# Optimization experiments

Hardware: AMD Instinct MI355X
Metric: run time of the kernel (lower is better)

## Reference

```python
import jax, jax.numpy as jnp
import numpy as np

BATCH, K, DIM = 512, 65536, 768

def _l2norm(x, axis=-1, eps=1e-12):
    return x / jnp.maximum(jnp.linalg.norm(x, axis=axis, keepdims=True), eps)

def setup_inputs() -> dict:
    key = jax.random.key(0)
    ks = jax.random.split(key, 8)
    s = 1.0 / np.sqrt(2 * DIM)
    return {
        "img_features": jax.random.normal(ks[0], (BATCH, DIM), jnp.float32),
        "txt_features": jax.random.normal(ks[1], (BATCH, DIM), jnp.float32),
        # queue buffers are L2-normalized at init in the torch module
        "queue_img": _l2norm(jax.random.normal(ks[2], (K, DIM), jnp.float32)),
        "queue_txt": _l2norm(jax.random.normal(ks[3], (K, DIM), jnp.float32)),
        "W_diff": jax.random.normal(ks[4], (2 * DIM, DIM), jnp.float32) * s,
        "b_diff": jnp.zeros((DIM,), jnp.float32),
        "W_comb": jax.random.normal(ks[5], (2 * DIM, DIM), jnp.float32) * s,
        "b_comb": jnp.zeros((DIM,), jnp.float32),
        "logit_scale": jnp.full((1,), 100.0, jnp.float32),  # clip logit_scale.exp()
    }

def reference(img_features, txt_features, queue_img, queue_txt,
              W_diff, b_diff, W_comb, b_comb, logit_scale):
    # normalize encoder outputs
    img_f = _l2norm(img_features)          # [n, c]
    txt_f = _l2norm(txt_features)          # [n, c]
    # brute-force cosine retrieval against the text queue
    retrieval_mat = jnp.einsum('nc,kc->nk', img_f, queue_txt)  # [n, K]
    ind_similar = jnp.argmax(retrieval_mat, axis=-1)           # [n]
    t_similar = queue_txt[ind_similar]                          # gather [n, c]
    # diff_net_q: concat -> linear -> relu
    diff = jax.nn.relu(jnp.concatenate([txt_f, t_similar], -1) @ W_diff + b_diff)
    # combine_net_q: concat -> linear
    combined = jnp.concatenate([img_f, diff], -1) @ W_comb + b_comb
    scale = jnp.mean(logit_scale)
    logits = scale * jnp.einsum('nc,kc->nk', combined, queue_img)  # [n, K]
    # dequeue/enqueue: scatter batch rows into the queue at ptr=0
    new_queue_img = jax.lax.dynamic_update_slice(queue_img, img_f, (0, 0))
    new_queue_txt = jax.lax.dynamic_update_slice(queue_txt, txt_f, (0, 0))
    return logits, ind_similar, new_queue_img, new_queue_txt
```

## Files before the change

### kernel.cpp

```cpp
#include <hip/hip_runtime.h>
#include <stdint.h>
#include <stddef.h>

#define BATCH 512
#define NQ    65536
#define DIM   768
#define DIM2  1536
#define CONVB 1024

typedef __attribute__((ext_vector_type(4))) float f32x4;
typedef __attribute__((ext_vector_type(4))) unsigned short u16x4;
typedef __attribute__((ext_vector_type(8))) unsigned short u16x8;
typedef __attribute__((ext_vector_type(8))) __bf16 bf16x8;

static __device__ __forceinline__ unsigned short f2bf(float x){
    unsigned int u = __float_as_uint(x);
    unsigned int r = ((u >> 16) & 1u) + 0x7fffu;
    return (unsigned short)((u + r) >> 16);
}
static __device__ __forceinline__ float bf2f(unsigned short h){
    return __uint_as_float(((unsigned int)h) << 16);
}

struct T2 { float v1, v2; int i1, i2; };
static __device__ __forceinline__ void t2_add(T2& t, float v, int i){
    if (v > t.v1 || (v == t.v1 && i < t.i1)) { t.v2 = t.v1; t.i2 = t.i1; t.v1 = v; t.i1 = i; }
    else if (v > t.v2 || (v == t.v2 && i < t.i2)) { t.v2 = v; t.i2 = i; }
}
static __device__ __forceinline__ T2 t2_init(){ T2 t; t.v1 = -3.4e38f; t.v2 = -3.4e38f; t.i1 = 0x7fffffff; t.i2 = 0x7fffffff; return t; }

__global__ __launch_bounds__(256) void prep_all(
    const float* __restrict__ img, const float* __restrict__ txt,
    const float* __restrict__ qtxt, const float* __restrict__ qimg,
    const float* __restrict__ Wd, const float* __restrict__ Wc,
    unsigned short* __restrict__ bthi, unsigned short* __restrict__ bihi,
    float* __restrict__ img_f, float* __restrict__ txt_f,
    unsigned short* __restrict__ X2hi, unsigned short* __restrict__ X2lo,
    unsigned short* __restrict__ X1hi, unsigned short* __restrict__ X1lo,
    float* __restrict__ out2, float* __restrict__ out3,
    float* __restrict__ Td, float* __restrict__ Tc)
{
    __shared__ float tbuf[32][33];
    __shared__ float red[4];
    const int b = blockIdx.x;
    if (b < 2 * CONVB){
        const bool isT = (b < CONVB);
        const float* __restrict__ src = isT ? qtxt : qimg;
        unsigned short* __restrict__ hi = isT ? bthi : bihi;
        const int bb = isT ? b : b - CONVB;
        const size_t n4 = (size_t)NQ * DIM / 4;
        for (size_t i = (size_t)bb * 256 + threadIdx.x; i < n4; i += (size_t)CONVB * 256){
            f32x4 v = ((const f32x4*)src)[i];
            u16x4 h;
            #pragma unroll
            for (int j = 0; j < 4; j++) h[j] = f2bf(v[j]);
            *(u16x4*)(hi + 4*i) = h;
        }
    } else if (b < 2 * CONVB + 2 * BATCH){
        const int b2 = b - 2 * CONVB;
        const bool isimg = (b2 < BATCH);
        const int row = isimg ? b2 : b2 - BATCH;
        const float* src = (isimg ? img : txt) + (size_t)row * DIM;
        float v[3];
        float ss = 0.f;
        #pragma unroll
        for (int i = 0; i < 3; i++){ v[i] = src[threadIdx.x + i*256]; ss += v[i]*v[i]; }
        #pragma unroll
        for (int m = 1; m < 64; m <<= 1) ss += __shfl_xor(ss, m);
        if ((threadIdx.x & 63) == 0) red[threadIdx.x >> 6] = ss;
        __syncthreads();
        float tot = red[0] + red[1] + red[2] + red[3];
        float scale = 1.0f / fmaxf(sqrtf(tot), 1e-12f);
        float* fdst = (isimg ? img_f : txt_f) + (size_t)row * DIM;
        float* odst = (isimg ? out2  : out3 ) + (size_t)row * DIM;
        unsigned short* hid = (isimg ? X2hi : X1hi) + (size_t)row * DIM2;
        unsigned short* lod = (isimg ? X2lo : X1lo) + (size_t)row * DIM2;
        #pragma unroll
        for (int i = 0; i < 3; i++){
            int c = threadIdx.x + i*256;
            float y = v[i] * scale;
            fdst[c] = y; odst[c] = y;
            unsigned short h = f2bf(y);
            hid[c] = h; lod[c] = f2bf(y - bf2f(h));
        }
    } else {
        int t = b - 2 * CONVB - 2 * BATCH;
        const int z = t / 1152; t -= z * 1152;
        const int x = t % 24, y = t / 24;
        const float* W = z ? Wc : Wd;
        float*       T = z ? Tc : Td;
        const int x0 = x * 32, y0 = y * 32;
        const int tx = threadIdx.x & 31, ty = threadIdx.x >> 5;
        #pragma unroll
        for (int i = 0; i < 32; i += 8)
            tbuf[ty + i][tx] = W[(size_t)(y0 + ty + i) * DIM + x0 + tx];
        __syncthreads();
        #pragma unroll
        for (int i = 0; i < 32; i += 8)
            T[(size_t)(x0 + ty + i) * DIM2 + y0 + tx] = tbuf[tx][ty + i];
    }
}

#define EPI_TOP2      0
#define EPI_BIAS_RELU 1
#define EPI_BIAS      2
#define EPI_SCALE     3

template<int EPI, bool WT>
__global__ __launch_bounds__(512, 2) void gemm_big(
    const unsigned short* __restrict__ Ahi, const unsigned short* __restrict__ Alo, int lda,
    const unsigned short* __restrict__ Bhi, const unsigned short* __restrict__ Blo, int ldb,
    int K, int Nout,
    float* __restrict__ outp, const float* __restrict__ scale_ptr, int Mtot,
    float* __restrict__ wt_out)
{
    constexpr int NT = 512;
    constexpr int KS = 64;
    constexpr int HT = 16384;
    constexpr int BUF = 4 * HT;
    __shared__ __align__(16) char lds[2 * BUF];

    const int tid = threadIdx.x, lane = tid & 63, wid = tid >> 6;
    const int wm = wid >> 2, wn = wid & 3;
    const int lr = lane & 15, lg = lane >> 4;
    const int id = blockIdx.x;
    const int l  = (id & 7) * 64 + (id >> 3);
    const int nb = l >> 1, mb = l & 1;
    const int m0 = mb * 256, n0 = nb * 256;

    f32x4 acc[8][4] = {};

    auto stageHT = [&](int T){
        int kind = T & 3, ks = T >> 2;
        char* base = lds + (ks & 1) * BUF + kind * HT;
        const unsigned short* hi = (kind < 2) ? Ahi : Bhi;
        const unsigned short* lo = (kind < 2) ? Alo : Blo;
        int ld = (kind < 2) ? lda : ldb;
        int r0 = ((kind < 2) ? m0 : n0) + (kind & 1) * 128;
        int k0 = ks * KS;
        #pragma unroll
        for (int r = 0; r < 2; r++){
            int G = r * NT + tid, row = G >> 3, slot = G & 7, s0 = slot ^ (row & 7);
            const unsigned short* s = ((s0 < 4) ? hi : lo) + (size_t)(r0 + row) * ld + k0 + (s0 & 3) * 8;
            __builtin_amdgcn_global_load_lds(
                (const __attribute__((address_space(1))) void*)s,
                (__attribute__((address_space(3))) void*)(base + (r * NT + (tid & ~63)) * 16), 16, 0, 0);
        }
    };

    const int xh = (lg ^ (lr & 7)) << 4;
    const int xl = ((4 + lg) ^ (lr & 7)) << 4;

    const int nk = K / KS;
    stageHT(0); stageHT(1); stageHT(2); stageHT(3);
    if (nk > 1){
        stageHT(6); stageHT(7);
        asm volatile("s_waitcnt vmcnt(4)" ::: "memory");
    } else {
        asm volatile("s_waitcnt vmcnt(0)" ::: "memory");
    }
    __syncthreads();

    for (int kt = 0; kt < nk; kt++){
        const char* Ab = lds + (kt & 1) * BUF;
        const char* Bb = Ab + 2 * HT;
        bf16x8 bh[4], bl[4];
        #pragma unroll
        for (int q = 0; q < 4; q++){
            if (q < 2){ if (kt + 1 < nk) stageHT(4 * (kt + 1) + q); }
            else      { if (kt + 2 < nk) stageHT(4 * (kt + 2) + q); }
            if (q == 0){
                #pragma unroll
                for (int nf = 0; nf < 4; nf++){
                    const char* rp = Bb + (wn * 64 + nf * 16 + lr) * 128;
                    bh[nf] = *(const bf16x8*)(rp + xh);
                    bl[nf] = *(const bf16x8*)(rp + xl);
                }
            }
            const char* rp0 = Ab + (wm * 128 + q * 32 + lr) * 128;
            const char* rp1 = rp0 + 16 * 128;
            bf16x8 a0h = *(const bf16x8*)(rp0 + xh);
            bf16x8 a0l = *(const bf16x8*)(rp0 + xl);
            bf16x8 a1h = *(const bf16x8*)(rp1 + xh);
            bf16x8 a1l = *(const bf16x8*)(rp1 + xl);
            asm volatile("s_barrier" ::: "memory");
            asm volatile("s_waitcnt lgkmcnt(0)" ::: "memory");
            __builtin_amdgcn_sched_barrier(0);
            __builtin_amdgcn_s_setprio(1);
            #pragma unroll
            for (int nf = 0; nf < 4; nf++)
                acc[2*q  ][nf] = __builtin_amdgcn_mfma_f32_16x16x32_bf16(a0h, bh[nf], acc[2*q  ][nf], 0, 0, 0);
            #pragma unroll
            for (int nf = 0; nf < 4; nf++)
                acc[2*q+1][nf] = __builtin_amdgcn_mfma_f32_16x16x32_bf16(a1h, bh[nf], acc[2*q+1][nf], 0, 0, 0);
            #pragma unroll
            for (int nf = 0; nf < 4; nf++)
                acc[2*q  ][nf] = __builtin_amdgcn_mfma_f32_16x16x32_bf16(a0l, bl[nf], acc[2*q  ][nf], 0, 0, 0);
            #pragma unroll
            for (int nf = 0; nf < 4; nf++)
                acc[2*q+1][nf] = __builtin_amdgcn_mfma_f32_16x16x32_bf16(a1l, bl[nf], acc[2*q+1][nf], 0, 0, 0);
            __builtin_amdgcn_s_setprio(0);
            if (q == 3){
                if (kt < nk - 2)       asm volatile("s_waitcnt vmcnt(4)" ::: "memory");
                else if (kt == nk - 2) asm volatile("s_waitcnt vmcnt(0)" ::: "memory");
            }
            asm volatile("s_barrier" ::: "memory");
        }
    }

    if constexpr (EPI == EPI_TOP2){
        T2* t2l = (T2*)lds;
        #pragma unroll
        for (int mf = 0; mf < 8; mf++){
            #pragma unroll
            for (int r = 0; r < 4; r++){
                T2 t = t2_init();
                #pragma unroll
                for (int nf = 0; nf < 4; nf++){
                    int gc = n0 + wn * 64 + nf * 16 + lr;
                    t2_add(t, acc[mf][nf][r], gc);
                }
                #pragma unroll
                for (int m = 1; m < 16; m <<= 1){
                    float ov1 = __shfl_xor(t.v1, m), ov2 = __shfl_xor(t.v2, m);
                    int   oi1 = __shfl_xor(t.i1, m), oi2 = __shfl_xor(t.i2, m);
                    t2_add(t, ov1, oi1); t2_add(t, ov2, oi2);
                }
                if (lr == 0){
                    int rowit = wm * 128 + mf * 16 + lg * 4 + r;
                    t2l[wn * 256 + rowit] = t;
                }
            }
        }
        __syncthreads();
        if (tid < 256){
            T2 t = t2l[tid];
            #pragma unroll
            for (int w = 1; w < 4; w++){
                T2 o = t2l[w * 256 + tid];
                t2_add(t, o.v1, o.i1); t2_add(t, o.v2, o.i2);
            }
            f32x4 pk; pk[0] = t.v1; pk[1] = __int_as_float(t.i1); pk[2] = t.v2; pk[3] = __int_as_float(t.i2);
            ((f32x4*)outp)[(size_t)nb * Mtot + (m0 + tid)] = pk;
        }
    } else if constexpr (EPI == EPI_SCALE){
        float sc = scale_ptr[0];
        #pragma unroll
        for (int mf = 0; mf < 8; mf++)
        #pragma unroll
        for (int nf = 0; nf < 4; nf++)
        #pragma unroll
        for (int r = 0; r < 4; r++){
            int grow = m0 + wm * 128 + mf * 16 + lg * 4 + r;
            int gcol = n0 + wn * 64 + nf * 16 + lr;
            outp[(size_t)grow * Nout + gcol] = acc[mf][nf][r] * sc;
        }
    }

    if constexpr (WT){
        if (mb == 0){
            constexpr int PR = DIM / 8;
            for (int t = tid; t < 256 * PR; t += NT){
                int r = n0 + t / PR;
                if (r >= BATCH){
                    int c = (t % PR) * 8;
                    u16x8 hv = *(const u16x8*)(Bhi + (size_t)r * ldb + c);
                    f32x4 f0, f1;
                    #pragma unroll
                    for (int j = 0; j < 4; j++){ f0[j] = bf2f(hv[j]); f1[j] = bf2f(hv[4 + j]); }
                    f32x4* wp = (f32x4*)(wt_out + (size_t)r * DIM + c);
                    wp[0] = f0; wp[1] = f1;
                }
            }
        }
    }
}

template<int BM,int BN,int WGM,int WGN,int EPI>
__global__ __launch_bounds__(WGM*WGN*64) void gemm_small(
    const unsigned short* __restrict__ Ahi, const unsigned short* __restrict__ Alo, int lda,
    const float* __restrict__ B, int ldb, int K,
    const float* __restrict__ bias,
    unsigned short* __restrict__ dsthi, unsigned short* __restrict__ dstlo, int ldd, int dstoff)
{
    constexpr int WM = BM / WGM, WN = BN / WGN;
    constexpr int MF = WM / 16, NF = WN / 16;
    constexpr int NT = WGM * WGN * 64;
    constexpr int ABYTES = BM * 128;
    constexpr int BBYTES = BN * 128;
    constexpr int BUF = ABYTES + BBYTES;
    static_assert(BN * 4 == NT, "");
    static_assert((BM * 8) % NT == 0, "");

    __shared__ __align__(16) char lds[2 * BUF];

    const int tid  = threadIdx.x;
    const int wid  = tid >> 6, lane = tid & 63;
    const int wm   = wid / WGN, wn = wid % WGN;
    const int lr   = lane & 15, lg = lane >> 4;
    const int nb   = blockIdx.x, mb = blockIdx.y;
    const int m0   = mb * BM, n0 = nb * BN;

    f32x4 acc[MF][NF] = {};
    f32x4 breg0, breg1;

    auto stageA = [&](int buf, int k0){
        char* base = lds + buf * BUF;
        constexpr int RA = BM * 8 / NT;
        #pragma unroll
        for (int r = 0; r < RA; r++){
            int G = r * NT + tid;
            int row = G >> 3, slot = G & 7;
            int s0 = slot ^ (row & 7);
            const unsigned short* src = ((s0 < 4) ? Ahi : Alo)
                + (size_t)(m0 + row) * lda + (k0 + (s0 & 3) * 8);
            char* ldst = base + r * NT * 16 + (tid & ~63) * 16;
            __builtin_amdgcn_global_load_lds(
                (const __attribute__((address_space(1))) void*)src,
                (__attribute__((address_space(3))) void*)ldst, 16, 0, 0);
        }
    };
    auto loadB = [&](int kt){
        int k0 = kt * 32;
        int row = tid >> 2, quad = tid & 3;
        const float* bp = B + (size_t)(n0 + row) * ldb + k0 + quad * 8;
        breg0 = *(const f32x4*)bp;
        breg1 = *(const f32x4*)(bp + 4);
    };
    auto writeB = [&](int buf){
        char* base = lds + buf * BUF + ABYTES;
        int row = tid >> 2, quad = tid & 3;
        u16x8 h8, l8;
        #pragma unroll
        for (int j = 0; j < 8; j++){
            float x = (j < 4) ? breg0[j] : breg1[j - 4];
            unsigned short h = f2bf(x);
            h8[j] = h; l8[j] = f2bf(x - bf2f(h));
        }
        int sh = quad ^ (row & 7), sl = (4 + quad) ^ (row & 7);
        *(u16x8*)(base + row * 128 + sh * 16) = h8;
        *(u16x8*)(base + row * 128 + sl * 16) = l8;
    };
    auto compute = [&](int buf){
        const char* Ab = lds + buf * BUF;
        const char* Bb = Ab + ABYTES;
        bf16x8 ah[MF], al[MF], bh[NF], bl[NF];
        #pragma unroll
        for (int mf = 0; mf < MF; mf++){
            int row = wm * WM + mf * 16 + lr;
            const char* rp = Ab + row * 128;
            ah[mf] = *(const bf16x8*)(rp + ((lg ^ (row & 7)) << 4));
            al[mf] = *(const bf16x8*)(rp + (((4 + lg) ^ (row & 7)) << 4));
        }
        #pragma unroll
        for (int nf = 0; nf < NF; nf++){
            int row = wn * WN + nf * 16 + lr;
            const char* rp = Bb + row * 128;
            bh[nf] = *(const bf16x8*)(rp + ((lg ^ (row & 7)) << 4));
            bl[nf] = *(const bf16x8*)(rp + (((4 + lg) ^ (row & 7)) << 4));
        }
        #pragma unroll
        for (int mf = 0; mf < MF; mf++)
        #pragma unroll
        for (int nf = 0; nf < NF; nf++){
            acc[mf][nf] = __builtin_amdgcn_mfma_f32_16x16x32_bf16(ah[mf], bh[nf], acc[mf][nf], 0, 0, 0);
            acc[mf][nf] = __builtin_amdgcn_mfma_f32_16x16x32_bf16(al[mf], bh[nf], acc[mf][nf], 0, 0, 0);
            acc[mf][nf] = __builtin_amdgcn_mfma_f32_16x16x32_bf16(ah[mf], bl[nf], acc[mf][nf], 0, 0, 0);
        }
    };

    stageA(0, 0); loadB(0); writeB(0);
    __syncthreads();
    const int nk = K / 32;
    int cur = 0;
    for (int kt = 0; kt < nk; kt++){
        if (kt + 1 < nk){ stageA(cur ^ 1, (kt + 1) * 32); loadB(kt + 1); }
        compute(cur);
        if (kt + 1 < nk){ writeB(cur ^ 1); }
        __syncthreads();
        cur ^= 1;
    }

    #pragma unroll
    for (int mf = 0; mf < MF; mf++)
    #pragma unroll
    for (int nf = 0; nf < NF; nf++)
    #pragma unroll
    for (int r = 0; r < 4; r++){
        int grow = m0 + wm * WM + mf * 16 + lg * 4 + r;
        int gcol = n0 + wn * WN + nf * 16 + lr;
        float c = acc[mf][nf][r] + bias[gcol];
        if (EPI == EPI_BIAS_RELU) c = fmaxf(c, 0.f);
        unsigned short h = f2bf(c);
        size_t o = (size_t)grow * ldd + dstoff + gcol;
        dsthi[o] = h;
        dstlo[o] = f2bf(c - bf2f(h));
    }
}

__global__ __launch_bounds__(256) void phaseB_kernel(
    const f32x4* __restrict__ top2ws, int ntiles,
    const float* __restrict__ img_f, const float* __restrict__ qtxt,
    float* __restrict__ out_ind,
    unsigned short* __restrict__ X1hi, unsigned short* __restrict__ X1lo)
{
    __shared__ float vals[512];
    __shared__ int   inds[512];
    __shared__ float red[4];
    __shared__ int   redi[4];
    __shared__ int   cands[4];
    __shared__ float cscore[4];
    __shared__ int   finali;
    const int row = blockIdx.x, tid = threadIdx.x;

    if (tid < ntiles){
        f32x4 e = top2ws[(size_t)tid * BATCH + row];
        vals[2*tid]   = e[0]; inds[2*tid]   = __float_as_int(e[1]);
        vals[2*tid+1] = e[2]; inds[2*tid+1] = __float_as_int(e[3]);
    }
    __syncthreads();

    for (int it = 0; it < 4; it++){
        float v = vals[tid]; int i = inds[tid];
        {
            float v2 = vals[tid+256]; int i2 = inds[tid+256];
            if (v2 > v || (v2 == v && i2 < i)){ v = v2; i = i2; }
        }
        #pragma unroll
        for (int m = 1; m < 64; m <<= 1){
            float ov = __shfl_xor(v, m); int oi = __shfl_xor(i, m);
            if (ov > v || (ov == v && oi < i)){ v = ov; i = oi; }
        }
        if ((tid & 63) == 0){ red[tid>>6] = v; redi[tid>>6] = i; }
        __syncthreads();
        if (tid == 0){
            float bv = red[0]; int bi = redi[0];
            #pragma unroll
            for (int w = 1; w < 4; w++)
                if (red[w] > bv || (red[w] == bv && redi[w] < bi)){ bv = red[w]; bi = redi[w]; }
            cands[it] = bi;
        }
        __syncthreads();
        if (inds[tid]     == cands[it]) vals[tid]     = -3.4e38f;
        if (inds[tid+256] == cands[it]) vals[tid+256] = -3.4e38f;
        __syncthreads();
    }

    const float* a = img_f + (size_t)row * DIM;
    float a0 = a[tid], a1 = a[tid + 256], a2 = a[tid + 512];
    for (int c = 0; c < 4; c++){
        const float* bp = qtxt + (size_t)cands[c] * DIM;
        float s = a0 * bp[tid] + a1 * bp[tid + 256] + a2 * bp[tid + 512];
        #pragma unroll
        for (int m = 1; m < 64; m <<= 1) s += __shfl_xor(s, m);
        if ((tid & 63) == 0) red[tid>>6] = s;
        __syncthreads();
        if (tid == 0) cscore[c] = red[0] + red[1] + red[2] + red[3];
        __syncthreads();
    }
    if (tid == 0){
        float bs = cscore[0]; int bi = cands[0];
        #pragma unroll
        for (int c = 1; c < 4; c++)
            if (cscore[c] > bs || (cscore[c] == bs && cands[c] < bi)){ bs = cscore[c]; bi = cands[c]; }
        out_ind[row] = (float)bi;
        finali = bi;
    }
    __syncthreads();

    const float* src = qtxt + (size_t)finali * DIM;
    for (int c = tid; c < DIM; c += 256){
        float x = src[c];
        unsigned short h = f2bf(x);
        X1hi[(size_t)row * DIM2 + DIM + c] = h;
        X1lo[(size_t)row * DIM2 + DIM + c] = f2bf(x - bf2f(h));
    }
}

extern "C" void kernel_launch(void* const* d_in, const int* in_sizes, int n_in,
                              void* d_out, int out_size, void* d_ws, size_t ws_size,
                              hipStream_t stream)
{
    (void)in_sizes; (void)n_in; (void)out_size; (void)ws_size;
    const float* img  = (const float*)d_in[0];
    const float* txt  = (const float*)d_in[1];
    const float* qimg = (const float*)d_in[2];
    const float* qtxt = (const float*)d_in[3];
    const float* Wd   = (const float*)d_in[4];
    const float* bd   = (const float*)d_in[5];
    const float* Wc   = (const float*)d_in[6];
    const float* bc   = (const float*)d_in[7];
    const float* ls   = (const float*)d_in[8];

    float* out0 = (float*)d_out;
    float* out1 = out0 + (size_t)BATCH * NQ;
    float* out2 = out1 + BATCH;
    float* out3 = out2 + (size_t)NQ * DIM;

    char* w = (char*)d_ws;
    auto alloc = [&](size_t bytes){ char* p = w; w += (bytes + 255) & ~(size_t)255; return p; };
    unsigned short* X1hi  = (unsigned short*)alloc((size_t)BATCH * DIM2 * 2);
    unsigned short* X1lo  = (unsigned short*)alloc((size_t)BATCH * DIM2 * 2);
    unsigned short* X2hi  = (unsigned short*)alloc((size_t)BATCH * DIM2 * 2);
    unsigned short* X2lo  = (unsigned short*)alloc((size_t)BATCH * DIM2 * 2);
    unsigned short* combhi= (unsigned short*)alloc((size_t)BATCH * DIM * 2);
    unsigned short* comblo= (unsigned short*)alloc((size_t)BATCH * DIM * 2);
    float* img_f  = (float*)alloc((size_t)BATCH * DIM * 4);
    float* txt_f  = (float*)alloc((size_t)BATCH * DIM * 4);
    float* Td     = (float*)alloc((size_t)DIM * DIM2 * 4);
    float* Tc     = (float*)alloc((size_t)DIM * DIM2 * 4);
    float* top2ws = (float*)alloc((size_t)(NQ / 256) * BATCH * 16);
    unsigned short* Bt_hi = (unsigned short*)alloc((size_t)NQ * DIM * 2);
    unsigned short* Bi_hi = (unsigned short*)alloc((size_t)NQ * DIM * 2);

    prep_all<<<dim3(2 * CONVB + 2 * BATCH + 2304), dim3(256), 0, stream>>>(
        img, txt, qtxt, qimg, Wd, Wc, Bt_hi, Bi_hi,
        img_f, txt_f, X2hi, X2lo, X1hi, X1lo, out2, out3, Td, Tc);

    gemm_big<EPI_TOP2, true><<<dim3(512), dim3(512), 0, stream>>>(
        X2hi, X2hi + 32, DIM2, Bt_hi, Bt_hi + 32, DIM, DIM, NQ, top2ws, nullptr, BATCH, out3);

    phaseB_kernel<<<dim3(BATCH), dim3(256), 0, stream>>>(
        (const f32x4*)top2ws, NQ / 256, img_f, qtxt, out1, X1hi, X1lo);

    gemm_small<64,64,2,2,EPI_BIAS_RELU><<<dim3(DIM / 64, BATCH / 64), dim3(256), 0, stream>>>(
        X1hi, X1lo, DIM2, Td, DIM2, DIM2, bd, X2hi, X2lo, DIM2, DIM);

    gemm_small<64,64,2,2,EPI_BIAS><<<dim3(DIM / 64, BATCH / 64), dim3(256), 0, stream>>>(
        X2hi, X2lo, DIM2, Tc, DIM2, DIM2, bc, combhi, comblo, DIM, 0);

    gemm_big<EPI_SCALE, true><<<dim3(512), dim3(512), 0, stream>>>(
        combhi, combhi + 32, DIM, Bi_hi, Bi_hi + 32, DIM, DIM, NQ, out0, ls, BATCH, out2);
}
```

Baseline: 570.6 us.

## Copy queue tails in bf16 conversion pass instead of GEMM epilogue

The rows of the new queue outputs that come after the batch are now written as exact fp32 copies from the source, using nontemporal stores, inside the prep kernel's bf16 conversion loop. Previously the GEMM epilogues wrote them by expanding bf16 values back to fp32. This removes a read of the bf16 queue and the tail work from both big GEMMs, and it also fixes the precision of those rows, which were truncated to bf16 before. The number of conversion blocks is doubled so that the extra stores in the prep stage get more parallelism.

```diff
diff --git a/kernel.cpp b/kernel.cpp
--- a/kernel.cpp
+++ b/kernel.cpp
@@ -6,7 +6,7 @@
 #define NQ    65536
 #define DIM   768
 #define DIM2  1536
-#define CONVB 1024
+#define CONVB 2048
 
 typedef __attribute__((ext_vector_type(4))) float f32x4;
 typedef __attribute__((ext_vector_type(4))) unsigned short u16x4;
@@ -46,11 +46,14 @@
     if (b < 2 * CONVB){
         const bool isT = (b < CONVB);
         const float* __restrict__ src = isT ? qtxt : qimg;
+        float* __restrict__ dst = isT ? out3 : out2;
         unsigned short* __restrict__ hi = isT ? bthi : bihi;
         const int bb = isT ? b : b - CONVB;
+        const size_t skip4 = (size_t)BATCH * DIM / 4;
         const size_t n4 = (size_t)NQ * DIM / 4;
         for (size_t i = (size_t)bb * 256 + threadIdx.x; i < n4; i += (size_t)CONVB * 256){
             f32x4 v = ((const f32x4*)src)[i];
+            if (i >= skip4) __builtin_nontemporal_store(v, (f32x4*)dst + i);
             u16x4 h;
             #pragma unroll
             for (int j = 0; j < 4; j++) h[j] = f2bf(v[j]);
@@ -106,13 +109,12 @@
 #define EPI_BIAS      2
 #define EPI_SCALE     3
 
-template<int EPI, bool WT>
+template<int EPI>
 __global__ __launch_bounds__(512, 2) void gemm_big(
     const unsigned short* __restrict__ Ahi, const unsigned short* __restrict__ Alo, int lda,
     const unsigned short* __restrict__ Bhi, const unsigned short* __restrict__ Blo, int ldb,
     int K, int Nout,
-    float* __restrict__ outp, const float* __restrict__ scale_ptr, int Mtot,
-    float* __restrict__ wt_out)
+    float* __restrict__ outp, const float* __restrict__ scale_ptr, int Mtot)
 {
     constexpr int NT = 512;
     constexpr int KS = 64;
@@ -256,24 +258,6 @@
             outp[(size_t)grow * Nout + gcol] = acc[mf][nf][r] * sc;
         }
     }
-
-    if constexpr (WT){
-        if (mb == 0){
-            constexpr int PR = DIM / 8;
-            for (int t = tid; t < 256 * PR; t += NT){
-                int r = n0 + t / PR;
-                if (r >= BATCH){
-                    int c = (t % PR) * 8;
-                    u16x8 hv = *(const u16x8*)(Bhi + (size_t)r * ldb + c);
-                    f32x4 f0, f1;
-                    #pragma unroll
-                    for (int j = 0; j < 4; j++){ f0[j] = bf2f(hv[j]); f1[j] = bf2f(hv[4 + j]); }
-                    f32x4* wp = (f32x4*)(wt_out + (size_t)r * DIM + c);
-                    wp[0] = f0; wp[1] = f1;
-                }
-            }
-        }
-    }
 }
 
 template<int BM,int BN,int WGM,int WGN,int EPI>
@@ -517,8 +501,8 @@
         img, txt, qtxt, qimg, Wd, Wc, Bt_hi, Bi_hi,
         img_f, txt_f, X2hi, X2lo, X1hi, X1lo, out2, out3, Td, Tc);
 
-    gemm_big<EPI_TOP2, true><<<dim3(512), dim3(512), 0, stream>>>(
-        X2hi, X2hi + 32, DIM2, Bt_hi, Bt_hi + 32, DIM, DIM, NQ, top2ws, nullptr, BATCH, out3);
+    gemm_big<EPI_TOP2><<<dim3(512), dim3(512), 0, stream>>>(
+        X2hi, X2hi + 32, DIM2, Bt_hi, Bt_hi + 32, DIM, DIM, NQ, top2ws, nullptr, BATCH);
 
     phaseB_kernel<<<dim3(BATCH), dim3(256), 0, stream>>>(
         (const f32x4*)top2ws, NQ / 256, img_f, qtxt, out1, X1hi, X1lo);
@@ -529,6 +513,6 @@
     gemm_small<64,64,2,2,EPI_BIAS><<<dim3(DIM / 64, BATCH / 64), dim3(256), 0, stream>>>(
         X2hi, X2lo, DIM2, Tc, DIM2, DIM2, bc, combhi, comblo, DIM, 0);
 
-    gemm_big<EPI_SCALE, true><<<dim3(512), dim3(512), 0, stream>>>(
-        combhi, combhi + 32, DIM, Bi_hi, Bi_hi + 32, DIM, DIM, NQ, out0, ls, BATCH, out2);
-}
+    gemm_big<EPI_SCALE><<<dim3(512), dim3(512), 0, stream>>>(
+        combhi, combhi + 32, DIM, Bi_hi, Bi_hi + 32, DIM, DIM, NQ, out0, ls, BATCH);
+}
```

After: 459.2 us, median of 2. 1.24x faster.
